# Kernel optimization log

Measured on AMD Instinct MI355X. Metric: run time of the kernel, lower is better.

The kernel has to match this reference:

```python
import jax, jax.numpy as jnp
import numpy as np

N, E = 50000, 800000
F_IN, HID, H, LBL = 512, 16, 8, 40
HC = HID * H  # 128
BN_EPS = 1e-5
ELU_ALPHA = 0.2
NEG_SLOPE = 0.2


def setup_inputs() -> dict:
    key = jax.random.key(0)
    ks = jax.random.split(key, 32)
    inp = {}
    inp['x'] = jax.random.normal(ks[0], (N, F_IN), dtype=jnp.float32)
    inp['edge_index'] = jax.random.randint(ks[1], (2, E), 0, N, dtype=jnp.int32)
    # layer 0: F_IN -> (H, HID), concat
    inp['W0'] = jax.random.normal(ks[2], (F_IN, HC), dtype=jnp.float32) * 0.05
    inp['as0'] = jax.random.normal(ks[3], (H, HID), dtype=jnp.float32) * 0.1
    inp['ad0'] = jax.random.normal(ks[4], (H, HID), dtype=jnp.float32) * 0.1
    inp['b0'] = jnp.zeros((HC,), jnp.float32)
    inp['g0'] = jnp.ones((HC,), jnp.float32)
    inp['be0'] = jnp.zeros((HC,), jnp.float32)
    inp['rm0'] = jnp.zeros((HC,), jnp.float32)
    inp['rv0'] = jnp.ones((HC,), jnp.float32)
    # layer 1: HC -> (H, HID), concat
    inp['W1'] = jax.random.normal(ks[5], (HC, HC), dtype=jnp.float32) * 0.1
    inp['as1'] = jax.random.normal(ks[6], (H, HID), dtype=jnp.float32) * 0.1
    inp['ad1'] = jax.random.normal(ks[7], (H, HID), dtype=jnp.float32) * 0.1
    inp['b1'] = jnp.zeros((HC,), jnp.float32)
    inp['g1'] = jnp.ones((HC,), jnp.float32)
    inp['be1'] = jnp.zeros((HC,), jnp.float32)
    inp['rm1'] = jnp.zeros((HC,), jnp.float32)
    inp['rv1'] = jnp.ones((HC,), jnp.float32)
    # layer 2: HC -> (1, LBL), mean (concat=False)
    inp['W2'] = jax.random.normal(ks[8], (HC, LBL), dtype=jnp.float32) * 0.1
    inp['as2'] = jax.random.normal(ks[9], (1, LBL), dtype=jnp.float32) * 0.1
    inp['ad2'] = jax.random.normal(ks[10], (1, LBL), dtype=jnp.float32) * 0.1
    inp['b2'] = jnp.zeros((LBL,), jnp.float32)
    return inp


def _gat_conv(xf, src, dst, W, a_src, a_dst, b, heads, out_ch, concat):
    # PyG GATConv (eval): linear -> per-head attn logits -> segment softmax over dst -> scatter-add
    n = xf.shape[0]
    h = (xf @ W).reshape(n, heads, out_ch)            # [N,H,C]
    alpha_s = jnp.einsum('nhc,hc->nh', h, a_src)      # [N,H]
    alpha_d = jnp.einsum('nhc,hc->nh', h, a_dst)
    e = jax.nn.leaky_relu(alpha_s[src] + alpha_d[dst], NEG_SLOPE)  # [Etot,H]
    m = jax.ops.segment_max(e, dst, num_segments=n)
    e = jnp.exp(e - m[dst])
    s = jax.ops.segment_sum(e, dst, num_segments=n)
    alpha = e / (s[dst] + 1e-16)                      # [Etot,H]
    msg = alpha[:, :, None] * h[src]                  # [Etot,H,C]
    out = jax.ops.segment_sum(msg, dst, num_segments=n)  # [N,H,C]
    out = out.reshape(n, heads * out_ch) if concat else out.mean(axis=1)
    return out + b


def _bn_elu(xf, g, be, rm, rv):
    y = (xf - rm) * (g * jax.lax.rsqrt(rv + BN_EPS)) + be
    return jnp.where(y > 0, y, ELU_ALPHA * jnp.expm1(y))


def reference(x, edge_index, W0, as0, ad0, b0, g0, be0, rm0, rv0,
              W1, as1, ad1, b1, g1, be1, rm1, rv1, W2, as2, ad2, b2):
    n = x.shape[0]
    # add self-loops (PyG GATConv default add_self_loops=True)
    loops = jnp.arange(n, dtype=edge_index.dtype)
    src = jnp.concatenate([edge_index[0], loops])
    dst = jnp.concatenate([edge_index[1], loops])
    h = _gat_conv(x, src, dst, W0, as0, ad0, b0, H, HID, True)
    h = _bn_elu(h, g0, be0, rm0, rv0)
    h = _gat_conv(h, src, dst, W1, as1, ad1, b1, H, HID, True)
    h = _bn_elu(h, g1, be1, rm1, rv1)
    out = _gat_conv(h, src, dst, W2, as2, ad2, b2, 1, LBL, False)
    return out
```

## Files before the change

kernel.cpp:

```cpp
#include <hip/hip_runtime.h>
#include <hip/hip_bf16.h>
#include <cstdint>
#include <cstddef>

#define NN 50000
#define EE 800000
#define FIN 512
#define HIDC 16
#define NH 8
#define HCH 128
#define NLBL 40
#define NLBLP 48
#define ETOT (EE + NN)
#define NEG_SLOPE 0.2f
#define ELU_A 0.2f
#define BN_EPS 1e-5f

typedef __attribute__((ext_vector_type(8))) short bf16x8;
typedef __attribute__((ext_vector_type(4))) short bf16x4;
typedef __attribute__((ext_vector_type(4))) float f32x4;

__device__ inline short f2b(float f) {
    __hip_bfloat16 h = __float2bfloat16(f);
    return *reinterpret_cast<short*>(&h);
}
__device__ inline float blo(unsigned int u) {
    union { unsigned int u; float f; } v; v.u = u << 16; return v.f;
}
__device__ inline float bhi(unsigned int u) {
    union { unsigned int u; float f; } v; v.u = u & 0xffff0000u; return v.f;
}

__global__ __launch_bounds__(256) void k_convW(const float* __restrict__ W,
                                               short* __restrict__ Wt,
                                               int K, int N, int Np)
{
    int idx = blockIdx.x * blockDim.x + threadIdx.x;
    if (idx >= Np * K) return;
    int n = idx / K, k = idx - n * K;
    float v = (n < N) ? W[(size_t)k * N + n] : 0.f;
    Wt[idx] = f2b(v);
}

template<int KDIM, bool A_BF16>
__global__ __launch_bounds__(512, 4) void k_gemm2(const void* __restrict__ Ap,
                                                  const short* __restrict__ Wt,
                                                  short* __restrict__ C,
                                                  int M)
{
    constexpr int KCH  = 128;
    constexpr int NCH  = KDIM / KCH;
    constexpr int LROW = KCH + 8;
    __shared__ short As[64 * LROW];
    __shared__ short Bs[128 * LROW];

    const int tid  = threadIdx.x;
    const int wv   = tid >> 6;
    const int lane = tid & 63;
    const int quad = lane >> 4;
    const int col  = lane & 15;
    const int wr   = wv >> 1;
    const int wn   = wv & 1;
    const int rowbase = blockIdx.x * 64;

    const float* Af = (const float*)Ap;
    const short* Ab = (const short*)Ap;

    float4 pa[4];
    bf16x8 pab[2];
    bf16x8 pb[4];

    auto loadA = [&](int c) {
        if constexpr (A_BF16) {
            #pragma unroll
            for (int r = 0; r < 2; ++r) {
                int gr = rowbase + r * 32 + (tid >> 4);
                gr = gr < M ? gr : M - 1;
                pab[r] = *(const bf16x8*)(Ab + (size_t)gr * KDIM + c * KCH + (tid & 15) * 8);
            }
        } else {
            #pragma unroll
            for (int r = 0; r < 4; ++r) {
                int gr = rowbase + r * 16 + (tid >> 5);
                gr = gr < M ? gr : M - 1;
                pa[r] = *(const float4*)(Af + (size_t)gr * KDIM + c * KCH + (tid & 31) * 4);
            }
        }
    };
    auto loadB = [&](int c) {
        #pragma unroll
        for (int r = 0; r < 4; ++r) {
            int n = r * 32 + (tid >> 4);
            pb[r] = *(const bf16x8*)(Wt + (size_t)n * KDIM + c * KCH + (tid & 15) * 8);
        }
    };
    auto writeAB = [&]() {
        if constexpr (A_BF16) {
            #pragma unroll
            for (int r = 0; r < 2; ++r) {
                int row = r * 32 + (tid >> 4);
                *(bf16x8*)(As + row * LROW + (tid & 15) * 8) = pab[r];
            }
        } else {
            #pragma unroll
            for (int r = 0; r < 4; ++r) {
                int row = r * 16 + (tid >> 5);
                bf16x4 w;
                w[0] = f2b(pa[r].x); w[1] = f2b(pa[r].y);
                w[2] = f2b(pa[r].z); w[3] = f2b(pa[r].w);
                *(bf16x4*)(As + row * LROW + (tid & 31) * 4) = w;
            }
        }
        #pragma unroll
        for (int r = 0; r < 4; ++r) {
            int n = r * 32 + (tid >> 4);
            *(bf16x8*)(Bs + n * LROW + (tid & 15) * 8) = pb[r];
        }
    };

    f32x4 acc[4];
    #pragma unroll
    for (int t = 0; t < 4; ++t) acc[t] = (f32x4){0.f, 0.f, 0.f, 0.f};

    loadA(0); loadB(0);

    for (int c = 0; c < NCH; ++c) {
        writeAB();
        __syncthreads();
        if (c + 1 < NCH) { loadA(c + 1); loadB(c + 1); }
        #pragma unroll
        for (int s = 0; s < KCH / 32; ++s) {
            bf16x8 af = *(const bf16x8*)(As + (wr * 16 + col) * LROW + s * 32 + quad * 8);
            #pragma unroll
            for (int t = 0; t < 4; ++t) {
                bf16x8 bf = *(const bf16x8*)(Bs + (wn * 64 + t * 16 + col) * LROW + s * 32 + quad * 8);
                acc[t] = __builtin_amdgcn_mfma_f32_16x16x32_bf16(af, bf, acc[t], 0, 0, 0);
            }
        }
        if (c + 1 < NCH) __syncthreads();
    }

    const int mb = rowbase + wr * 16 + quad * 4;
    #pragma unroll
    for (int t = 0; t < 4; ++t) {
        int cc = wn * 64 + t * 16 + col;
        #pragma unroll
        for (int r = 0; r < 4; ++r) {
            int m = mb + r;
            if (m < M) C[(size_t)m * HCH + cc] = f2b(acc[t][r]);
        }
    }
}

template<int KDIM, int NTILES, bool A_BF16>
__global__ __launch_bounds__(256) void k_gemm_lds(const void* __restrict__ Ap,
                                                  const short* __restrict__ Wt,
                                                  short* __restrict__ C,
                                                  int M, int N)
{
    constexpr int NFULL = NTILES * 16;
    constexpr int KCH = 128;
    constexpr int NK = KDIM / 32;
    constexpr int NCH = KDIM / KCH;
    constexpr int LROW = KCH + 8;
    __shared__ short Bs[NFULL * LROW];

    const int tid  = threadIdx.x;
    const int wave = tid >> 6;
    const int lane = tid & 63;
    const int quad = lane >> 4;
    const int col  = lane & 15;
    const int cb   = blockIdx.y * NFULL;
    const int row  = blockIdx.x * 64 + wave * 16 + col;
    const int arow = row < M ? row : M - 1;

    f32x4 acc[NTILES];
    #pragma unroll
    for (int t = 0; t < NTILES; ++t) acc[t] = (f32x4){0.f, 0.f, 0.f, 0.f};

    bf16x8 arB[4];
    float4 arF[4][2];
    const short* Ab = (const short*)Ap;
    const float* Af = (const float*)Ap;
    auto pf = [&](int ks) {
        if (ks >= NK) return;
        if (A_BF16) {
            arB[ks & 3] = *(const bf16x8*)(Ab + (size_t)arow * KDIM + ks * 32 + quad * 8);
        } else {
            const float4* p = (const float4*)(Af + (size_t)arow * KDIM + ks * 32 + quad * 8);
            arF[ks & 3][0] = p[0];
            arF[ks & 3][1] = p[1];
        }
    };
    pf(0); pf(1); pf(2); pf(3);

    for (int c = 0; c < NCH; ++c) {
        const int k0 = c * KCH;
        constexpr int TOT8 = NFULL * (KCH / 8);
        #pragma unroll
        for (int i = tid; i < TOT8; i += 256) {
            int n  = i >> 4;
            int kk = i & 15;
            bf16x8 v = *(const bf16x8*)(Wt + (size_t)(cb + n) * KDIM + k0 + kk * 8);
            *(bf16x8*)(Bs + n * LROW + kk * 8) = v;
        }
        __syncthreads();
        #pragma unroll
        for (int s = 0; s < KCH / 32; ++s) {
            const int ks = c * (KCH / 32) + s;
            bf16x8 afrag;
            if (A_BF16) {
                afrag = arB[ks & 3];
            } else {
                float4 v0 = arF[ks & 3][0], v1 = arF[ks & 3][1];
                afrag[0] = f2b(v0.x); afrag[1] = f2b(v0.y);
                afrag[2] = f2b(v0.z); afrag[3] = f2b(v0.w);
                afrag[4] = f2b(v1.x); afrag[5] = f2b(v1.y);
                afrag[6] = f2b(v1.z); afrag[7] = f2b(v1.w);
            }
            pf(ks + 4);
            #pragma unroll
            for (int t = 0; t < NTILES; ++t) {
                bf16x8 bfrag = *(const bf16x8*)(Bs + (t * 16 + col) * LROW + s * 32 + quad * 8);
                acc[t] = __builtin_amdgcn_mfma_f32_16x16x32_bf16(afrag, bfrag, acc[t], 0, 0, 0);
            }
        }
        if (c + 1 < NCH) __syncthreads();
    }

    const int mbase = blockIdx.x * 64 + wave * 16 + quad * 4;
    #pragma unroll
    for (int t = 0; t < NTILES; ++t) {
        int cc = cb + t * 16 + col;
        if (cc < N) {
            #pragma unroll
            for (int r = 0; r < 4; ++r) {
                int m = mbase + r;
                if (m < M) C[(size_t)m * N + cc] = f2b(acc[t][r]);
            }
        }
    }
}

__global__ __launch_bounds__(256) void k_alpha(const unsigned short* __restrict__ h,
                                               const float* __restrict__ a_s,
                                               const float* __restrict__ a_d,
                                               float* __restrict__ as_o,
                                               float* __restrict__ ad_o)
{
    int idx = blockIdx.x * blockDim.x + threadIdx.x;
    if (idx >= NN * NH) return;
    int hh = idx & (NH - 1);
    const uint4* hp = (const uint4*)(h + (size_t)idx * HIDC);
    uint4 q0 = hp[0], q1 = hp[1];
    unsigned int u[8] = {q0.x, q0.y, q0.z, q0.w, q1.x, q1.y, q1.z, q1.w};
    const float* ap = a_s + hh * HIDC;
    const float* dp = a_d + hh * HIDC;
    float ss = 0.f, dd = 0.f;
    #pragma unroll
    for (int i = 0; i < 8; ++i) {
        float f0 = blo(u[i]), f1 = bhi(u[i]);
        ss += f0 * ap[2 * i] + f1 * ap[2 * i + 1];
        dd += f0 * dp[2 * i] + f1 * dp[2 * i + 1];
    }
    as_o[idx] = ss;
    ad_o[idx] = dd;
}

__global__ __launch_bounds__(256) void k_alpha2(const unsigned short* __restrict__ h2,
                                                const float* __restrict__ a_s,
                                                const float* __restrict__ a_d,
                                                float* __restrict__ as_o,
                                                float* __restrict__ ad_o)
{
    int n = blockIdx.x * blockDim.x + threadIdx.x;
    if (n >= NN) return;
    const uint4* hp = (const uint4*)(h2 + (size_t)n * NLBL);
    float ss = 0.f, dd = 0.f;
    #pragma unroll
    for (int qi = 0; qi < 5; ++qi) {
        uint4 q = hp[qi];
        unsigned int u[4] = {q.x, q.y, q.z, q.w};
        #pragma unroll
        for (int j = 0; j < 4; ++j) {
            int c = qi * 8 + j * 2;
            float f0 = blo(u[j]), f1 = bhi(u[j]);
            ss += f0 * a_s[c] + f1 * a_s[c + 1];
            dd += f0 * a_d[c] + f1 * a_d[c + 1];
        }
    }
    as_o[n] = ss;
    ad_o[n] = dd;
}

__global__ __launch_bounds__(256) void k_hist(const int* __restrict__ ei,
                                              int* __restrict__ deg)
{
    int e = blockIdx.x * blockDim.x + threadIdx.x;
    if (e >= ETOT) return;
    int dst = (e < EE) ? ei[EE + e] : (e - EE);
    atomicAdd(&deg[dst], 1);
}

__global__ __launch_bounds__(1024) void k_scan(const int* __restrict__ deg,
                                               int* __restrict__ row_ptr,
                                               int* __restrict__ cursor)
{
    __shared__ int sm[1024];
    __shared__ int carry;
    int tid = threadIdx.x;
    if (tid == 0) carry = 0;
    __syncthreads();
    for (int base = 0; base < NN; base += 8192) {
        int v[8];
        int s = 0;
        int i0 = base + tid * 8;
        #pragma unroll
        for (int j = 0; j < 8; ++j) {
            int i = i0 + j;
            v[j] = (i < NN) ? deg[i] : 0;
            s += v[j];
        }
        sm[tid] = s;
        __syncthreads();
        for (int ofs = 1; ofs < 1024; ofs <<= 1) {
            int t = (tid >= ofs) ? sm[tid - ofs] : 0;
            __syncthreads();
            sm[tid] += t;
            __syncthreads();
        }
        int excl = sm[tid] - s + carry;
        #pragma unroll
        for (int j = 0; j < 8; ++j) {
            int i = i0 + j;
            if (i < NN) { row_ptr[i] = excl; cursor[i] = excl; }
            excl += v[j];
        }
        int total = sm[1023];
        __syncthreads();
        if (tid == 0) carry += total;
        __syncthreads();
    }
    if (tid == 0) row_ptr[NN] = carry;
}

__global__ __launch_bounds__(256) void k_scatter(const int* __restrict__ ei,
                                                 int* __restrict__ cursor,
                                                 int* __restrict__ csr_src)
{
    int e = blockIdx.x * blockDim.x + threadIdx.x;
    if (e >= ETOT) return;
    int src, dst;
    if (e < EE) { src = ei[e]; dst = ei[EE + e]; }
    else        { src = dst = e - EE; }
    int pos = atomicAdd(&cursor[dst], 1);
    csr_src[pos] = src;
}

__global__ __launch_bounds__(256) void k_agg(const int* __restrict__ row_ptr,
                                             const int* __restrict__ csr_src,
                                             const unsigned short* __restrict__ h,
                                             const float* __restrict__ as,
                                             const float* __restrict__ ad,
                                             const float* __restrict__ b,
                                             const float* __restrict__ g,
                                             const float* __restrict__ be,
                                             const float* __restrict__ rm,
                                             const float* __restrict__ rv,
                                             short* __restrict__ out)
{
    int n = blockIdx.x * 4 + (threadIdx.x >> 6);
    if (n >= NN) return;
    int lane = threadIdx.x & 63;
    int half = lane >> 5;
    int c4 = lane & 31;
    int hh = c4 >> 2;
    float adv = ad[n * NH + hh];
    float a0 = 0.f, a1 = 0.f, a2 = 0.f, a3 = 0.f, sw = 0.f;
    int jb = row_ptr[n], je = row_ptr[n + 1];
    int j = jb + half;
    for (; j + 6 < je; j += 8) {
        int s0 = csr_src[j];
        int s1 = csr_src[j + 2];
        int s2 = csr_src[j + 4];
        int s3 = csr_src[j + 6];
        float l0 = as[s0 * NH + hh] + adv;
        float l1 = as[s1 * NH + hh] + adv;
        float l2 = as[s2 * NH + hh] + adv;
        float l3 = as[s3 * NH + hh] + adv;
        uint2 u0 = *(const uint2*)(h + (size_t)s0 * HCH + 4 * c4);
        uint2 u1 = *(const uint2*)(h + (size_t)s1 * HCH + 4 * c4);
        uint2 u2 = *(const uint2*)(h + (size_t)s2 * HCH + 4 * c4);
        uint2 u3 = *(const uint2*)(h + (size_t)s3 * HCH + 4 * c4);
        l0 = l0 > 0.f ? l0 : NEG_SLOPE * l0;
        l1 = l1 > 0.f ? l1 : NEG_SLOPE * l1;
        l2 = l2 > 0.f ? l2 : NEG_SLOPE * l2;
        l3 = l3 > 0.f ? l3 : NEG_SLOPE * l3;
        float w0 = __expf(l0), w1 = __expf(l1), w2 = __expf(l2), w3 = __expf(l3);
        sw += (w0 + w1) + (w2 + w3);
        a0 += w0 * blo(u0.x) + w1 * blo(u1.x) + w2 * blo(u2.x) + w3 * blo(u3.x);
        a1 += w0 * bhi(u0.x) + w1 * bhi(u1.x) + w2 * bhi(u2.x) + w3 * bhi(u3.x);
        a2 += w0 * blo(u0.y) + w1 * blo(u1.y) + w2 * blo(u2.y) + w3 * blo(u3.y);
        a3 += w0 * bhi(u0.y) + w1 * bhi(u1.y) + w2 * bhi(u2.y) + w3 * bhi(u3.y);
    }
    for (; j < je; j += 2) {
        int s0 = csr_src[j];
        float l0 = as[s0 * NH + hh] + adv;
        uint2 u0 = *(const uint2*)(h + (size_t)s0 * HCH + 4 * c4);
        l0 = l0 > 0.f ? l0 : NEG_SLOPE * l0;
        float w0 = __expf(l0);
        sw += w0;
        a0 += w0 * blo(u0.x);
        a1 += w0 * bhi(u0.x);
        a2 += w0 * blo(u0.y);
        a3 += w0 * bhi(u0.y);
    }
    a0 += __shfl_down(a0, 32);
    a1 += __shfl_down(a1, 32);
    a2 += __shfl_down(a2, 32);
    a3 += __shfl_down(a3, 32);
    sw += __shfl_down(sw, 32);
    if (half == 0) {
        int c = 4 * c4;
        float inv = 1.f / (sw + 1e-16f);
        float4 bv  = *(const float4*)(b + c);
        float4 gv  = *(const float4*)(g + c);
        float4 bev = *(const float4*)(be + c);
        float4 rmv = *(const float4*)(rm + c);
        float4 rvv = *(const float4*)(rv + c);
        float r0 = a0 * inv + bv.x;
        float r1 = a1 * inv + bv.y;
        float r2 = a2 * inv + bv.z;
        float r3 = a3 * inv + bv.w;
        r0 = (r0 - rmv.x) * (gv.x * rsqrtf(rvv.x + BN_EPS)) + bev.x;
        r1 = (r1 - rmv.y) * (gv.y * rsqrtf(rvv.y + BN_EPS)) + bev.y;
        r2 = (r2 - rmv.z) * (gv.z * rsqrtf(rvv.z + BN_EPS)) + bev.z;
        r3 = (r3 - rmv.w) * (gv.w * rsqrtf(rvv.w + BN_EPS)) + bev.w;
        r0 = r0 > 0.f ? r0 : ELU_A * expm1f(r0);
        r1 = r1 > 0.f ? r1 : ELU_A * expm1f(r1);
        r2 = r2 > 0.f ? r2 : ELU_A * expm1f(r2);
        r3 = r3 > 0.f ? r3 : ELU_A * expm1f(r3);
        unsigned int lo = (unsigned int)(unsigned short)f2b(r0) |
                          ((unsigned int)(unsigned short)f2b(r1) << 16);
        unsigned int hi = (unsigned int)(unsigned short)f2b(r2) |
                          ((unsigned int)(unsigned short)f2b(r3) << 16);
        *(uint2*)(out + (size_t)n * HCH + c) = make_uint2(lo, hi);
    }
}

__global__ __launch_bounds__(256) void k_agg2(const int* __restrict__ row_ptr,
                                              const int* __restrict__ csr_src,
                                              const unsigned short* __restrict__ h2,
                                              const float* __restrict__ as,
                                              const float* __restrict__ ad,
                                              const float* __restrict__ b,
                                              float* __restrict__ out)
{
    int n = blockIdx.x * 4 + (threadIdx.x >> 6);
    if (n >= NN) return;
    int lane = threadIdx.x & 63;
    int half = lane >> 5;
    int c2 = lane & 31;
    bool act = c2 < 20;
    int coff = act ? 2 * c2 : 0;
    float adv = ad[n];
    float acc0 = 0.f, acc1 = 0.f, sw = 0.f;
    int jb = row_ptr[n], je = row_ptr[n + 1];
    int j = jb + half;
    for (; j + 6 < je; j += 8) {
        int s0 = csr_src[j];
        int s1 = csr_src[j + 2];
        int s2 = csr_src[j + 4];
        int s3 = csr_src[j + 6];
        float l0 = as[s0] + adv;
        float l1 = as[s1] + adv;
        float l2 = as[s2] + adv;
        float l3 = as[s3] + adv;
        unsigned int u0 = *(const unsigned int*)(h2 + (size_t)s0 * NLBL + coff);
        unsigned int u1 = *(const unsigned int*)(h2 + (size_t)s1 * NLBL + coff);
        unsigned int u2 = *(const unsigned int*)(h2 + (size_t)s2 * NLBL + coff);
        unsigned int u3 = *(const unsigned int*)(h2 + (size_t)s3 * NLBL + coff);
        l0 = l0 > 0.f ? l0 : NEG_SLOPE * l0;
        l1 = l1 > 0.f ? l1 : NEG_SLOPE * l1;
        l2 = l2 > 0.f ? l2 : NEG_SLOPE * l2;
        l3 = l3 > 0.f ? l3 : NEG_SLOPE * l3;
        float w0 = __expf(l0), w1 = __expf(l1), w2 = __expf(l2), w3 = __expf(l3);
        sw += (w0 + w1) + (w2 + w3);
        if (act) {
            acc0 += w0 * blo(u0) + w1 * blo(u1) + w2 * blo(u2) + w3 * blo(u3);
            acc1 += w0 * bhi(u0) + w1 * bhi(u1) + w2 * bhi(u2) + w3 * bhi(u3);
        }
    }
    for (; j < je; j += 2) {
        int s = csr_src[j];
        float l = as[s] + adv;
        unsigned int u = *(const unsigned int*)(h2 + (size_t)s * NLBL + coff);
        l = l > 0.f ? l : NEG_SLOPE * l;
        float w = __expf(l);
        sw += w;
        if (act) {
            acc0 += w * blo(u);
            acc1 += w * bhi(u);
        }
    }
    float acc0b = __shfl_down(acc0, 32);
    float acc1b = __shfl_down(acc1, 32);
    float swb   = __shfl_down(sw, 32);
    if (half == 0 && act) {
        acc0 += acc0b; acc1 += acc1b; sw += swb;
        float inv = 1.f / (sw + 1e-16f);
        out[(size_t)n * NLBL + 2 * c2]     = acc0 * inv + b[2 * c2];
        out[(size_t)n * NLBL + 2 * c2 + 1] = acc1 * inv + b[2 * c2 + 1];
    }
}

extern "C" void kernel_launch(void* const* d_in, const int* in_sizes, int n_in,
                              void* d_out, int out_size, void* d_ws, size_t ws_size,
                              hipStream_t stream)
{
    const float* x   = (const float*)d_in[0];
    const int*   ei  = (const int*)d_in[1];
    const float* W0  = (const float*)d_in[2];
    const float* as0 = (const float*)d_in[3];
    const float* ad0 = (const float*)d_in[4];
    const float* b0  = (const float*)d_in[5];
    const float* g0  = (const float*)d_in[6];
    const float* be0 = (const float*)d_in[7];
    const float* rm0 = (const float*)d_in[8];
    const float* rv0 = (const float*)d_in[9];
    const float* W1  = (const float*)d_in[10];
    const float* as1 = (const float*)d_in[11];
    const float* ad1 = (const float*)d_in[12];
    const float* b1  = (const float*)d_in[13];
    const float* g1  = (const float*)d_in[14];
    const float* be1 = (const float*)d_in[15];
    const float* rm1 = (const float*)d_in[16];
    const float* rv1 = (const float*)d_in[17];
    const float* W2  = (const float*)d_in[18];
    const float* a_s2 = (const float*)d_in[19];
    const float* a_d2 = (const float*)d_in[20];
    const float* b2  = (const float*)d_in[21];
    float* out = (float*)d_out;

    char* ws = (char*)d_ws;
    size_t off = 0;
    auto alloc = [&](size_t bytes) {
        void* p = (void*)(ws + off);
        off += (bytes + 255) & ~(size_t)255;
        return p;
    };
    short* hbuf   = (short*)alloc((size_t)NN * HCH * 2);
    short* fbuf   = (short*)alloc((size_t)NN * HCH * 2);
    float* asb    = (float*)alloc((size_t)NN * NH * 4);
    float* adb    = (float*)alloc((size_t)NN * NH * 4);
    int*   deg    = (int*)alloc((size_t)NN * 4);
    int*   rowp   = (int*)alloc((size_t)(NN + 1) * 4);
    int*   cursor = (int*)alloc((size_t)NN * 4);
    int*   csrs   = (int*)alloc((size_t)ETOT * 4);
    short* Wt0    = (short*)alloc((size_t)HCH * FIN * 2);
    short* Wt1    = (short*)alloc((size_t)HCH * HCH * 2);
    short* Wt2    = (short*)alloc((size_t)NLBLP * HCH * 2);
    short* h2     = hbuf;

    const int T = 256;
    const int gE  = (ETOT + T - 1) / T;
    const int gNH = (NN * NH + T - 1) / T;
    const int gN4 = (NN + 3) / 4;
    const int gM  = (NN + 63) / 64;

    k_convW<<<(HCH * FIN + T - 1) / T, T, 0, stream>>>(W0, Wt0, FIN, HCH, HCH);
    k_convW<<<(HCH * HCH + T - 1) / T, T, 0, stream>>>(W1, Wt1, HCH, HCH, HCH);
    k_convW<<<(NLBLP * HCH + T - 1) / T, T, 0, stream>>>(W2, Wt2, HCH, NLBL, NLBLP);

    hipMemsetAsync(deg, 0, (size_t)NN * 4, stream);
    k_hist<<<gE, T, 0, stream>>>(ei, deg);
    k_scan<<<1, 1024, 0, stream>>>(deg, rowp, cursor);
    k_scatter<<<gE, T, 0, stream>>>(ei, cursor, csrs);

    k_gemm2<FIN, false><<<gM, 512, 0, stream>>>(x, Wt0, hbuf, NN);
    k_alpha<<<gNH, T, 0, stream>>>((const unsigned short*)hbuf, as0, ad0, asb, adb);
    k_agg<<<gN4, T, 0, stream>>>(rowp, csrs, (const unsigned short*)hbuf, asb, adb,
                                 b0, g0, be0, rm0, rv0, fbuf);

    k_gemm2<HCH, true><<<gM, 512, 0, stream>>>(fbuf, Wt1, hbuf, NN);
    k_alpha<<<gNH, T, 0, stream>>>((const unsigned short*)hbuf, as1, ad1, asb, adb);
    k_agg<<<gN4, T, 0, stream>>>(rowp, csrs, (const unsigned short*)hbuf, asb, adb,
                                 b1, g1, be1, rm1, rv1, fbuf);

    k_gemm_lds<HCH, 3, true><<<dim3(gM, 1), T, 0, stream>>>(fbuf, Wt2, h2, NN, NLBL);
    k_alpha2<<<(NN + T - 1) / T, T, 0, stream>>>((const unsigned short*)h2, a_s2, a_d2, asb, adb);
    k_agg2<<<gN4, T, 0, stream>>>(rowp, csrs, (const unsigned short*)h2, asb, adb, b2, out);
}
```

Measured before the change: 465.1 us.

## Fuse attention logits into GEMM epilogues and merge preprocessing kernels

Computes the per-head source and destination attention logits inside the GEMM epilogues with lane shuffles, so the separate alpha kernels and their re-read of h are gone. The three weight conversions and the degree histogram are merged into one launch. The single-block scan is replaced by a three-stage multi-block scan. The CSR scatter now runs as extra blocks of the first GEMM so the two can overlap. This cuts launch count and serial work, but adds atomics contention alongside the GEMM, and the logits are now computed from fp32 accumulators rather than the bf16-rounded h.

```diff
diff --git a/kernel.cpp b/kernel.cpp
--- a/kernel.cpp
+++ b/kernel.cpp
@@ -15,6 +15,8 @@
 #define NEG_SLOPE 0.2f
 #define ELU_A 0.2f
 #define BN_EPS 1e-5f
+#define SCH 8192
+#define NCHK 7
 
 typedef __attribute__((ext_vector_type(8))) short bf16x8;
 typedef __attribute__((ext_vector_type(4))) short bf16x4;
@@ -31,23 +33,127 @@
     union { unsigned int u; float f; } v; v.u = u & 0xffff0000u; return v.f;
 }
 
-__global__ __launch_bounds__(256) void k_convW(const float* __restrict__ W,
-                                               short* __restrict__ Wt,
-                                               int K, int N, int Np)
-{
-    int idx = blockIdx.x * blockDim.x + threadIdx.x;
-    if (idx >= Np * K) return;
-    int n = idx / K, k = idx - n * K;
-    float v = (n < N) ? W[(size_t)k * N + n] : 0.f;
-    Wt[idx] = f2b(v);
-}
-
-template<int KDIM, bool A_BF16>
+__global__ __launch_bounds__(256) void k_prep(const float* __restrict__ W0, short* __restrict__ Wt0,
+                                              const float* __restrict__ W1, short* __restrict__ Wt1,
+                                              const float* __restrict__ W2, short* __restrict__ Wt2,
+                                              const int* __restrict__ ei, int* __restrict__ deg)
+{
+    int b = blockIdx.x;
+    int tid = threadIdx.x;
+    if (b < 256) {
+        int idx = b * 256 + tid;
+        int n = idx >> 9, k = idx & 511;
+        Wt0[idx] = f2b(W0[(size_t)k * HCH + n]);
+        return;
+    }
+    b -= 256;
+    if (b < 64) {
+        int idx = b * 256 + tid;
+        int n = idx >> 7, k = idx & 127;
+        Wt1[idx] = f2b(W1[(size_t)k * HCH + n]);
+        return;
+    }
+    b -= 64;
+    if (b < 24) {
+        int idx = b * 256 + tid;
+        int n = idx >> 7, k = idx & 127;
+        Wt2[idx] = f2b(n < NLBL ? W2[(size_t)k * NLBL + n] : 0.f);
+        return;
+    }
+    b -= 24;
+    {
+        int e = b * 256 + tid;
+        if (e < ETOT) {
+            int dst = (e < EE) ? ei[EE + e] : (e - EE);
+            atomicAdd(&deg[dst], 1);
+        }
+    }
+}
+
+__global__ __launch_bounds__(1024) void k_scan1(const int* __restrict__ deg,
+                                                int* __restrict__ row_ptr,
+                                                int* __restrict__ tot)
+{
+    __shared__ int sm[1024];
+    int b = blockIdx.x, tid = threadIdx.x;
+    int i0 = b * SCH + tid * 8;
+    int v[8];
+    int s = 0;
+    #pragma unroll
+    for (int j = 0; j < 8; ++j) {
+        int i = i0 + j;
+        v[j] = (i < NN) ? deg[i] : 0;
+        s += v[j];
+    }
+    sm[tid] = s;
+    __syncthreads();
+    for (int ofs = 1; ofs < 1024; ofs <<= 1) {
+        int t = (tid >= ofs) ? sm[tid - ofs] : 0;
+        __syncthreads();
+        sm[tid] += t;
+        __syncthreads();
+    }
+    int excl = sm[tid] - s;
+    #pragma unroll
+    for (int j = 0; j < 8; ++j) {
+        int i = i0 + j;
+        if (i < NN) row_ptr[i] = excl;
+        excl += v[j];
+    }
+    if (tid == 1023) tot[b] = sm[1023];
+}
+
+__global__ __launch_bounds__(64) void k_scan2(const int* __restrict__ tot,
+                                              int* __restrict__ totp,
+                                              int* __restrict__ row_ptr)
+{
+    if (threadIdx.x == 0) {
+        int run = 0;
+        for (int i = 0; i < NCHK; ++i) { totp[i] = run; run += tot[i]; }
+        row_ptr[NN] = run;
+    }
+}
+
+__global__ __launch_bounds__(256) void k_scan3(int* __restrict__ row_ptr,
+                                               int* __restrict__ cursor,
+                                               const int* __restrict__ totp)
+{
+    int i = blockIdx.x * 256 + threadIdx.x;
+    if (i < NN) {
+        int v = row_ptr[i] + totp[i / SCH];
+        row_ptr[i] = v;
+        cursor[i] = v;
+    }
+}
+
+constexpr int GM0 = (NN + 63) / 64;
+template<int KDIM, bool A_BF16, bool SCAT>
 __global__ __launch_bounds__(512, 4) void k_gemm2(const void* __restrict__ Ap,
                                                   const short* __restrict__ Wt,
                                                   short* __restrict__ C,
-                                                  int M)
-{
+                                                  int M,
+                                                  const float* __restrict__ a_s,
+                                                  const float* __restrict__ a_d,
+                                                  float* __restrict__ as_o,
+                                                  float* __restrict__ ad_o,
+                                                  const int* __restrict__ ei,
+                                                  int* __restrict__ cursor,
+                                                  int* __restrict__ csr_src)
+{
+    if constexpr (SCAT) {
+        if (blockIdx.x >= GM0) {
+            int e = (blockIdx.x - GM0) * 512 + threadIdx.x;
+            if (e < ETOT) {
+                int src, dst;
+                if (e < EE) { src = ei[e]; dst = ei[EE + e]; }
+                else        { src = dst = e - EE; }
+                int pos = atomicAdd(&cursor[dst], 1);
+                csr_src[pos] = src;
+            }
+            return;
+        }
+    }
+
     constexpr int KCH  = 128;
     constexpr int NCH  = KDIM / KCH;
     constexpr int LROW = KCH + 8;
@@ -141,6 +247,7 @@
     }
 
     const int mb = rowbase + wr * 16 + quad * 4;
+
     #pragma unroll
     for (int t = 0; t < 4; ++t) {
         int cc = wn * 64 + t * 16 + col;
@@ -148,6 +255,27 @@
         for (int r = 0; r < 4; ++r) {
             int m = mb + r;
             if (m < M) C[(size_t)m * HCH + cc] = f2b(acc[t][r]);
+        }
+    }
+
+    #pragma unroll
+    for (int t = 0; t < 4; ++t) {
+        int hh = wn * 4 + t;
+        float ws = a_s[hh * HIDC + col];
+        float wd = a_d[hh * HIDC + col];
+        #pragma unroll
+        for (int r = 0; r < 4; ++r) {
+            float vs = acc[t][r] * ws;
+            float vd = acc[t][r] * wd;
+            vs += __shfl_xor(vs, 1);  vd += __shfl_xor(vd, 1);
+            vs += __shfl_xor(vs, 2);  vd += __shfl_xor(vd, 2);
+            vs += __shfl_xor(vs, 4);  vd += __shfl_xor(vd, 4);
+            vs += __shfl_xor(vs, 8);  vd += __shfl_xor(vd, 8);
+            int m = mb + r;
+            if (col == 0 && m < M) {
+                as_o[m * NH + hh] = vs;
+                ad_o[m * NH + hh] = vd;
+            }
         }
     }
 }
@@ -156,7 +284,11 @@
 __global__ __launch_bounds__(256) void k_gemm_lds(const void* __restrict__ Ap,
                                                   const short* __restrict__ Wt,
                                                   short* __restrict__ C,
-                                                  int M, int N)
+                                                  int M, int N,
+                                                  const float* __restrict__ a_s2,
+                                                  const float* __restrict__ a_d2,
+                                                  float* __restrict__ as_o,
+                                                  float* __restrict__ ad_o)
 {
     constexpr int NFULL = NTILES * 16;
     constexpr int KCH = 128;
@@ -170,7 +302,6 @@
     const int lane = tid & 63;
     const int quad = lane >> 4;
     const int col  = lane & 15;
-    const int cb   = blockIdx.y * NFULL;
     const int row  = blockIdx.x * 64 + wave * 16 + col;
     const int arow = row < M ? row : M - 1;
 
@@ -201,7 +332,7 @@
         for (int i = tid; i < TOT8; i += 256) {
             int n  = i >> 4;
             int kk = i & 15;
-            bf16x8 v = *(const bf16x8*)(Wt + (size_t)(cb + n) * KDIM + k0 + kk * 8);
+            bf16x8 v = *(const bf16x8*)(Wt + (size_t)n * KDIM + k0 + kk * 8);
             *(bf16x8*)(Bs + n * LROW + kk * 8) = v;
         }
         __syncthreads();
@@ -231,7 +362,7 @@
     const int mbase = blockIdx.x * 64 + wave * 16 + quad * 4;
     #pragma unroll
     for (int t = 0; t < NTILES; ++t) {
-        int cc = cb + t * 16 + col;
+        int cc = t * 16 + col;
         if (cc < N) {
             #pragma unroll
             for (int r = 0; r < 4; ++r) {
@@ -240,121 +371,33 @@
             }
         }
     }
-}
-
-__global__ __launch_bounds__(256) void k_alpha(const unsigned short* __restrict__ h,
-                                               const float* __restrict__ a_s,
-                                               const float* __restrict__ a_d,
-                                               float* __restrict__ as_o,
-                                               float* __restrict__ ad_o)
-{
-    int idx = blockIdx.x * blockDim.x + threadIdx.x;
-    if (idx >= NN * NH) return;
-    int hh = idx & (NH - 1);
-    const uint4* hp = (const uint4*)(h + (size_t)idx * HIDC);
-    uint4 q0 = hp[0], q1 = hp[1];
-    unsigned int u[8] = {q0.x, q0.y, q0.z, q0.w, q1.x, q1.y, q1.z, q1.w};
-    const float* ap = a_s + hh * HIDC;
-    const float* dp = a_d + hh * HIDC;
-    float ss = 0.f, dd = 0.f;
-    #pragma unroll
-    for (int i = 0; i < 8; ++i) {
-        float f0 = blo(u[i]), f1 = bhi(u[i]);
-        ss += f0 * ap[2 * i] + f1 * ap[2 * i + 1];
-        dd += f0 * dp[2 * i] + f1 * dp[2 * i + 1];
-    }
-    as_o[idx] = ss;
-    ad_o[idx] = dd;
-}
-
-__global__ __launch_bounds__(256) void k_alpha2(const unsigned short* __restrict__ h2,
-                                                const float* __restrict__ a_s,
-                                                const float* __restrict__ a_d,
-                                                float* __restrict__ as_o,
-                                                float* __restrict__ ad_o)
-{
-    int n = blockIdx.x * blockDim.x + threadIdx.x;
-    if (n >= NN) return;
-    const uint4* hp = (const uint4*)(h2 + (size_t)n * NLBL);
-    float ss = 0.f, dd = 0.f;
-    #pragma unroll
-    for (int qi = 0; qi < 5; ++qi) {
-        uint4 q = hp[qi];
-        unsigned int u[4] = {q.x, q.y, q.z, q.w};
-        #pragma unroll
-        for (int j = 0; j < 4; ++j) {
-            int c = qi * 8 + j * 2;
-            float f0 = blo(u[j]), f1 = bhi(u[j]);
-            ss += f0 * a_s[c] + f1 * a_s[c + 1];
-            dd += f0 * a_d[c] + f1 * a_d[c + 1];
-        }
-    }
-    as_o[n] = ss;
-    ad_o[n] = dd;
-}
-
-__global__ __launch_bounds__(256) void k_hist(const int* __restrict__ ei,
-                                              int* __restrict__ deg)
-{
-    int e = blockIdx.x * blockDim.x + threadIdx.x;
-    if (e >= ETOT) return;
-    int dst = (e < EE) ? ei[EE + e] : (e - EE);
-    atomicAdd(&deg[dst], 1);
-}
-
-__global__ __launch_bounds__(1024) void k_scan(const int* __restrict__ deg,
-                                               int* __restrict__ row_ptr,
-                                               int* __restrict__ cursor)
-{
-    __shared__ int sm[1024];
-    __shared__ int carry;
-    int tid = threadIdx.x;
-    if (tid == 0) carry = 0;
-    __syncthreads();
-    for (int base = 0; base < NN; base += 8192) {
-        int v[8];
-        int s = 0;
-        int i0 = base + tid * 8;
-        #pragma unroll
-        for (int j = 0; j < 8; ++j) {
-            int i = i0 + j;
-            v[j] = (i < NN) ? deg[i] : 0;
-            s += v[j];
-        }
-        sm[tid] = s;
-        __syncthreads();
-        for (int ofs = 1; ofs < 1024; ofs <<= 1) {
-            int t = (tid >= ofs) ? sm[tid - ofs] : 0;
-            __syncthreads();
-            sm[tid] += t;
-            __syncthreads();
-        }
-        int excl = sm[tid] - s + carry;
-        #pragma unroll
-        for (int j = 0; j < 8; ++j) {
-            int i = i0 + j;
-            if (i < NN) { row_ptr[i] = excl; cursor[i] = excl; }
-            excl += v[j];
-        }
-        int total = sm[1023];
-        __syncthreads();
-        if (tid == 0) carry += total;
-        __syncthreads();
-    }
-    if (tid == 0) row_ptr[NN] = carry;
-}
-
-__global__ __launch_bounds__(256) void k_scatter(const int* __restrict__ ei,
-                                                 int* __restrict__ cursor,
-                                                 int* __restrict__ csr_src)
-{
-    int e = blockIdx.x * blockDim.x + threadIdx.x;
-    if (e >= ETOT) return;
-    int src, dst;
-    if (e < EE) { src = ei[e]; dst = ei[EE + e]; }
-    else        { src = dst = e - EE; }
-    int pos = atomicAdd(&cursor[dst], 1);
-    csr_src[pos] = src;
+
+    float vs[4] = {0.f, 0.f, 0.f, 0.f};
+    float vd[4] = {0.f, 0.f, 0.f, 0.f};
+    #pragma unroll
+    for (int t = 0; t < NTILES; ++t) {
+        int cc = t * 16 + col;
+        float ws = cc < NLBL ? a_s2[cc] : 0.f;
+        float wd = cc < NLBL ? a_d2[cc] : 0.f;
+        #pragma unroll
+        for (int r = 0; r < 4; ++r) {
+            vs[r] += acc[t][r] * ws;
+            vd[r] += acc[t][r] * wd;
+        }
+    }
+    #pragma unroll
+    for (int r = 0; r < 4; ++r) {
+        float s = vs[r], d = vd[r];
+        s += __shfl_xor(s, 1);  d += __shfl_xor(d, 1);
+        s += __shfl_xor(s, 2);  d += __shfl_xor(d, 2);
+        s += __shfl_xor(s, 4);  d += __shfl_xor(d, 4);
+        s += __shfl_xor(s, 8);  d += __shfl_xor(d, 8);
+        int m = mbase + r;
+        if (col == 0 && m < M) {
+            as_o[m] = s;
+            ad_o[m] = d;
+        }
+    }
 }
 
 __global__ __launch_bounds__(256) void k_agg(const int* __restrict__ row_ptr,
@@ -560,34 +603,36 @@
     short* Wt0    = (short*)alloc((size_t)HCH * FIN * 2);
     short* Wt1    = (short*)alloc((size_t)HCH * HCH * 2);
     short* Wt2    = (short*)alloc((size_t)NLBLP * HCH * 2);
+    int*   tot    = (int*)alloc(64 * 4);
+    int*   totp   = (int*)alloc(64 * 4);
     short* h2     = hbuf;
 
     const int T = 256;
-    const int gE  = (ETOT + T - 1) / T;
-    const int gNH = (NN * NH + T - 1) / T;
     const int gN4 = (NN + 3) / 4;
     const int gM  = (NN + 63) / 64;
-
-    k_convW<<<(HCH * FIN + T - 1) / T, T, 0, stream>>>(W0, Wt0, FIN, HCH, HCH);
-    k_convW<<<(HCH * HCH + T - 1) / T, T, 0, stream>>>(W1, Wt1, HCH, HCH, HCH);
-    k_convW<<<(NLBLP * HCH + T - 1) / T, T, 0, stream>>>(W2, Wt2, HCH, NLBL, NLBLP);
+    const int gPrep = 256 + 64 + 24 + (ETOT + T - 1) / T;
+    const int gScat = (ETOT + 511) / 512;
 
     hipMemsetAsync(deg, 0, (size_t)NN * 4, stream);
-    k_hist<<<gE, T, 0, stream>>>(ei, deg);
-    k_scan<<<1, 1024, 0, stream>>>(deg, rowp, cursor);
-    k_scatter<<<gE, T, 0, stream>>>(ei, cursor, csrs);
-
-    k_gemm2<FIN, false><<<gM, 512, 0, stream>>>(x, Wt0, hbuf, NN);
-    k_alpha<<<gNH, T, 0, stream>>>((const unsigned short*)hbuf, as0, ad0, asb, adb);
+    k_prep<<<gPrep, T, 0, stream>>>(W0, Wt0, W1, Wt1, W2, Wt2, ei, deg);
+
+    k_scan1<<<NCHK, 1024, 0, stream>>>(deg, rowp, tot);
+    k_scan2<<<1, 64, 0, stream>>>(tot, totp, rowp);
+    k_scan3<<<(NN + T - 1) / T, T, 0, stream>>>(rowp, cursor, totp);
+
+    k_gemm2<FIN, false, true><<<gM + gScat, 512, 0, stream>>>(x, Wt0, hbuf, NN,
+                                                              as0, ad0, asb, adb,
+                                                              ei, cursor, csrs);
     k_agg<<<gN4, T, 0, stream>>>(rowp, csrs, (const unsigned short*)hbuf, asb, adb,
                                  b0, g0, be0, rm0, rv0, fbuf);
 
-    k_gemm2<HCH, true><<<gM, 512, 0, stream>>>(fbuf, Wt1, hbuf, NN);
-    k_alpha<<<gNH, T, 0, stream>>>((const unsigned short*)hbuf, as1, ad1, asb, adb);
+    k_gemm2<HCH, true, false><<<gM, 512, 0, stream>>>(fbuf, Wt1, hbuf, NN,
+                                                      as1, ad1, asb, adb,
+                                                      nullptr, nullptr, nullptr);
     k_agg<<<gN4, T, 0, stream>>>(rowp, csrs, (const unsigned short*)hbuf, asb, adb,
                                  b1, g1, be1, rm1, rv1, fbuf);
 
-    k_gemm_lds<HCH, 3, true><<<dim3(gM, 1), T, 0, stream>>>(fbuf, Wt2, h2, NN, NLBL);
-    k_alpha2<<<(NN + T - 1) / T, T, 0, stream>>>((const unsigned short*)h2, a_s2, a_d2, asb, adb);
+    k_gemm_lds<HCH, 3, true><<<gM, T, 0, stream>>>(fbuf, Wt2, h2, NN, NLBL,
+                                                   a_s2, a_d2, asb, adb);
     k_agg2<<<gN4, T, 0, stream>>>(rowp, csrs, (const unsigned short*)h2, asb, adb, b2, out);
 }
```

Result: no change. 458.4 us (-1.4%).
